# Kernel optimization log

Hardware: AMD Instinct MI355X
Metric: run time of the kernel (lower is better)

## Reference

```python
import jax, jax.numpy as jnp
import numpy as np

B, C, HH, WW, HEADS = 4, 64, 256, 256, 8
CH = C // HEADS              # 8 per-head dim
HID = int(C * 2.66)          # 170
EPS_LN = 1e-5
EPS = 1e-6
QK_NORM = 1.0
# crpe windows for 8 heads: {3:2, 5:3, 7:3}; each conv input split = head_split*Ch*2
WINDOWS = [(3, 2), (5, 3), (7, 3)]


def conv2d(x, w, b=None, groups=1, pad=0):
    out = jax.lax.conv_general_dilated(
        x, w, (1, 1), [(pad, pad), (pad, pad)],
        dimension_numbers=('NCHW', 'OIHW', 'NCHW'), feature_group_count=groups)
    return out if b is None else out + b[None, :, None, None]


def setup_inputs() -> dict:
    key = jax.random.key(0)
    ks = jax.random.split(key, 32)
    p = lambda k, shp, s=0.05: jax.random.normal(k, shp, jnp.float32) * s
    inp = {
        'x': jax.random.normal(ks[0], (B, HH * WW, C), jnp.float32),
        'ln1_w': jnp.ones((C,), jnp.float32) + p(ks[1], (C,), 0.01),
        'sca_w': p(ks[2], (C, C, 1, 1)), 'sca_b': p(ks[3], (C,)),
        'dw1_w': p(ks[4], (2 * C, C, 1, 1)),          # 1x1 dim->2dim
        'dw2_w': p(ks[5], (C, 2, 3, 3)),              # grouped 3x3, groups=C, in/grp=2
        'qkv_w': p(ks[6], (3 * C, C, 1, 1)),
        'qkv_dw_w': p(ks[7], (3 * C, 1, 3, 3)),       # depthwise 3x3
        'temperature': jnp.ones((HEADS, 1, 1), jnp.float32),
        'r3_w': p(ks[8], (2, 2 * CH, 3, 3)), 'r3_b': p(ks[9], (2,)),
        'r5_w': p(ks[10], (3, 2 * CH, 5, 5)), 'r5_b': p(ks[11], (3,)),
        'r7_w': p(ks[12], (3, 2 * CH, 7, 7)), 'r7_b': p(ks[13], (3,)),
        'proj_w': p(ks[14], (C, C, 1, 1)),
        'ln2_w': jnp.ones((C,), jnp.float32) + p(ks[15], (C,), 0.01),
        'pin_w': p(ks[16], (2 * HID, C, 1, 1)),
        'ffn_dw_w': p(ks[17], (2 * HID, 1, 3, 3)),
        'pout_w': p(ks[18], (C, HID, 1, 1)),
        'H': HH, 'W': WW,
    }
    return inp


def biasfree_ln(x, w):
    # BiasFree LayerNorm over channel dim of NCHW (var only, no mean-subtract)
    sigma = jnp.var(x, axis=1, keepdims=True)
    return x / jnp.sqrt(sigma + EPS_LN) * w[None, :, None, None]


def refine_att(q, k, H, W, convs):
    # q: (B,h,N,Ch)  k: (B,h,Ch,N) -> per-head conv relative position map (B,h,N,1)
    b, h, N, Ch = q.shape
    q_img = q.transpose(0, 1, 3, 2).reshape(b, h, Ch, H, W)
    k_img = k.reshape(b, h, Ch, H, W)
    qk = jnp.concatenate([q_img, k_img], axis=2).reshape(b, h * 2 * Ch, H, W)
    splits = np.cumsum([s * 2 * Ch for _, s in WINDOWS])[:-1]
    parts = jnp.split(qk, splits, axis=1)
    outs = [conv2d(xp, wt, bs, groups=g, pad=win // 2)
            for (win, g), (wt, bs), xp in zip(WINDOWS, convs, parts)]
    att = jnp.concatenate(outs, axis=1)           # (b, h, H, W)
    return att.reshape(b, h, 1, H * W).transpose(0, 1, 3, 2)  # (b,h,N,1)


def attention(x, sca_w, sca_b, dw1_w, dw2_w, qkv_w, qkv_dw_w, temperature,
              refine_convs, proj_w, H, W):
    b, c, _, _ = x.shape
    N = H * W
    xsca = conv2d(jnp.mean(x, axis=(2, 3), keepdims=True), sca_w, sca_b)
    x1 = conv2d(conv2d(x, dw1_w), dw2_w, groups=c, pad=1)
    qkv = conv2d(conv2d(x, qkv_w), qkv_dw_w, groups=3 * c, pad=1)
    q, k, v = jnp.split(qkv, 3, axis=1)
    q = q.reshape(b, HEADS, CH, N).transpose(0, 1, 3, 2)  # b h N Ch
    k = k.reshape(b, HEADS, CH, N)                        # b h Ch N
    v = v.reshape(b, HEADS, CH, N).transpose(0, 1, 3, 2)  # b h N Ch
    q = q / (jnp.linalg.norm(q, axis=-1, keepdims=True) / QK_NORM + EPS)
    k = k / (jnp.linalg.norm(k, axis=-2, keepdims=True) / QK_NORM + EPS)
    refine_w = jax.nn.sigmoid(refine_att(q, k, H, W, refine_convs))
    attn = k @ v                                           # b h Ch Ch
    out_num = jnp.sum(v, axis=-2, keepdims=True) + q @ attn
    ksum = jnp.sum(k, axis=-1, keepdims=True)              # b h Ch 1
    out_den = jnp.asarray(N, q.dtype) + q @ ksum + EPS     # b h N 1 (bcast to Ch)
    out = out_num / out_den * temperature
    out = out * refine_w
    out = out.transpose(0, 1, 3, 2).reshape(b, c, H, W)
    out = out * xsca * jax.nn.gelu(x1, approximate=False)
    return conv2d(out, proj_w)


def feedforward(x, pin_w, ffn_dw_w, pout_w):
    h = conv2d(x, pin_w)
    h = conv2d(h, ffn_dw_w, groups=2 * HID, pad=1)
    h1, h2 = jnp.split(h, 2, axis=1)
    return conv2d(jax.nn.gelu(h1, approximate=False) * h2, pout_w)


def reference(x, ln1_w, sca_w, sca_b, dw1_w, dw2_w, qkv_w, qkv_dw_w, temperature,
              r3_w, r3_b, r5_w, r5_b, r7_w, r7_b, proj_w, ln2_w,
              pin_w, ffn_dw_w, pout_w, H, W):
    b = x.shape[0]
    xi = x.reshape(b, H, W, C).transpose(0, 3, 1, 2)  # NCHW
    refine_convs = [(r3_w, r3_b), (r5_w, r5_b), (r7_w, r7_b)]
    xi = xi + attention(biasfree_ln(xi, ln1_w), sca_w, sca_b, dw1_w, dw2_w,
                        qkv_w, qkv_dw_w, temperature, refine_convs, proj_w, H, W)
    xi = xi + feedforward(biasfree_ln(xi, ln2_w), pin_w, ffn_dw_w, pout_w)
    return xi
```

## Files before the change

kernel.cpp:

```cpp
#include <hip/hip_runtime.h>
#include <math.h>
#include <stdio.h>

#define BB 4
#define NP 65536

typedef unsigned short u16;
typedef unsigned int u32;
typedef __attribute__((ext_vector_type(8))) short short8;
typedef __attribute__((ext_vector_type(4))) float f32x4;
typedef __attribute__((ext_vector_type(2))) float f32x2;

__device__ __forceinline__ float bf2f(u16 u) { return __uint_as_float((u32)u << 16); }
__device__ __forceinline__ u16 f2bf(float f) {
  u32 u = __float_as_uint(f);
  u = (u + 0x7FFFu + ((u >> 16) & 1u)) >> 16;
  return (u16)u;
}
__device__ __forceinline__ float gelu_f(float x) {
  return 0.5f * x * (1.f + erff(x * 0.70710678118654752f));
}
__device__ __forceinline__ float wlo(u32 w) { return __uint_as_float(w << 16); }
__device__ __forceinline__ float whi(u32 w) { return __uint_as_float(w & 0xFFFF0000u); }

__global__ __launch_bounds__(256) void k_ln1(const float* __restrict__ x,
                                             u16* __restrict__ xb1,
                                             float* __restrict__ meanraw) {
  int t = threadIdx.x;
  int b = blockIdx.y;
  int lane = t & 63;
  int cg = t & 15;
  float a0 = 0.f, a1 = 0.f, a2 = 0.f, a3 = 0.f;
#pragma unroll
  for (int it = 0; it < 8; it++) {
    long px = (long)blockIdx.x * 128 + (t >> 4) + it * 16;
    const float* xr = x + ((long)b * NP + px) * 64 + cg * 4;
    float4 v = *(const float4*)(xr);
    float s1 = v.x + v.y + v.z + v.w;
    float s2 = v.x * v.x + v.y * v.y + v.z * v.z + v.w * v.w;
    s1 += __shfl_xor(s1, 1); s2 += __shfl_xor(s2, 1);
    s1 += __shfl_xor(s1, 2); s2 += __shfl_xor(s2, 2);
    s1 += __shfl_xor(s1, 4); s2 += __shfl_xor(s2, 4);
    s1 += __shfl_xor(s1, 8); s2 += __shfl_xor(s2, 8);
    float m = s1 * (1.f / 64.f);
    float var = s2 * (1.f / 64.f) - m * m;
    float sg = rsqrtf(var + 1e-5f);
    float h0 = v.x * sg, h1 = v.y * sg, h2 = v.z * sg, h3 = v.w * sg;
    uint2 pk;
    pk.x = (u32)f2bf(h0) | ((u32)f2bf(h1) << 16);
    pk.y = (u32)f2bf(h2) | ((u32)f2bf(h3) << 16);
    *(uint2*)(xb1 + ((long)b * NP + px) * 64 + cg * 4) = pk;
    a0 += h0; a1 += h1; a2 += h2; a3 += h3;
  }
  a0 += __shfl_xor(a0, 16); a1 += __shfl_xor(a1, 16);
  a2 += __shfl_xor(a2, 16); a3 += __shfl_xor(a3, 16);
  a0 += __shfl_xor(a0, 32); a1 += __shfl_xor(a1, 32);
  a2 += __shfl_xor(a2, 32); a3 += __shfl_xor(a3, 32);
  __shared__ float cm[64];
  if (t < 64) cm[t] = 0.f;
  __syncthreads();
  if (lane < 16) {
    atomicAdd(&cm[cg * 4 + 0], a0);
    atomicAdd(&cm[cg * 4 + 1], a1);
    atomicAdd(&cm[cg * 4 + 2], a2);
    atomicAdd(&cm[cg * 4 + 3], a3);
  }
  __syncthreads();
  if (t < 64) atomicAdd(&meanraw[b * 64 + t], cm[t]);
}

__global__ void k_xsca(const float* __restrict__ meanraw, const float* __restrict__ lnw,
                       const float* __restrict__ sca_w, const float* __restrict__ sca_b,
                       float* __restrict__ xsca) {
  int t = threadIdx.x;
  int b = t >> 6, co = t & 63;
  float a = sca_b[co];
  for (int ci = 0; ci < 64; ci++)
    a += sca_w[co * 64 + ci] * meanraw[b * 64 + ci] * lnw[ci] * (1.f / 65536.f);
  xsca[t] = a;
}

__global__ void k_foldW1b(const float* __restrict__ qkv_w, const float* __restrict__ dw1_w,
                          const float* __restrict__ lnw, u16* __restrict__ W1b) {
  int i = blockIdx.x * 256 + threadIdx.x;
  if (i < 320 * 64) {
    int co = i >> 6, ci = i & 63;
    float w = (co < 192) ? qkv_w[co * 64 + ci] : dw1_w[(co - 192) * 64 + ci];
    W1b[i] = f2bf(w * lnw[ci]);
  }
}
__global__ void k_foldW2b(const float* __restrict__ pin_w, const float* __restrict__ lnw,
                          u16* __restrict__ W2b) {
  int i = blockIdx.x * 256 + threadIdx.x;
  if (i < 384 * 64) {
    int co = i >> 6, ci = i & 63;
    float v = 0.f;
    if (co < 340) {
      int pair = co >> 1, which = co & 1;
      v = pin_w[(pair + which * 170) * 64 + ci] * lnw[ci];
    }
    W2b[i] = f2bf(v);
  }
}
__global__ void k_foldWpb(const float* __restrict__ w, u16* __restrict__ Wpb) {
  int i = blockIdx.x * 256 + threadIdx.x;
  if (i < 4096) Wpb[i] = f2bf(w[i]);
}
__global__ void k_tpoutb(const float* __restrict__ w, u16* __restrict__ Wob) {
  int i = blockIdx.x * 256 + threadIdx.x;
  if (i < 64 * 192) {
    int co = i / 192, ci = i - co * 192;
    Wob[i] = (ci < 170) ? f2bf(w[co * 170 + ci]) : (u16)0;
  }
}

template <int EPI>
__global__ __launch_bounds__(256) void k_mgemm(const u16* __restrict__ in, long in_bs,
                                               const u16* __restrict__ W,
                                               u16* __restrict__ outp, long out_bs,
                                               const float* __restrict__ xres,
                                               float* __restrict__ xo,
                                               u16* __restrict__ xb2r) {
  int t = threadIdx.x;
  int lane = t & 63, wv = t >> 6;
  int l15 = lane & 15, quad = lane >> 4;
  int pxw = blockIdx.x * 256 + wv * 64;
  int co0 = blockIdx.y * 64;
  int b = blockIdx.z;
  const u16* inb = in + (long)b * in_bs;

  short8 aw[4][2];
#pragma unroll
  for (int t4 = 0; t4 < 4; t4++)
#pragma unroll
    for (int kf = 0; kf < 2; kf++)
      aw[t4][kf] = *(const short8*)(W + (long)(co0 + t4 * 16 + l15) * 64 + kf * 32 + quad * 8);

  f32x4 acc[4][4];
#pragma unroll
  for (int t4 = 0; t4 < 4; t4++)
#pragma unroll
    for (int p = 0; p < 4; p++) acc[t4][p] = (f32x4){0.f, 0.f, 0.f, 0.f};

#pragma unroll
  for (int p = 0; p < 4; p++) {
    long px = pxw + p * 16 + l15;
    short8 bf0 = *(const short8*)(inb + px * 64 + quad * 8);
    short8 bf1 = *(const short8*)(inb + px * 64 + 32 + quad * 8);
#pragma unroll
    for (int t4 = 0; t4 < 4; t4++) {
      acc[t4][p] = __builtin_amdgcn_mfma_f32_16x16x32_bf16(aw[t4][0], bf0, acc[t4][p], 0, 0, 0);
      acc[t4][p] = __builtin_amdgcn_mfma_f32_16x16x32_bf16(aw[t4][1], bf1, acc[t4][p], 0, 0, 0);
    }
  }

  if (EPI == 0) {
    u16* ob = outp + (long)b * out_bs;
#pragma unroll
    for (int t4 = 0; t4 < 4; t4++)
#pragma unroll
      for (int p = 0; p < 4; p++) {
#pragma unroll
        for (int reg = 0; reg < 4; reg++) {
          int co = co0 + t4 * 16 + quad * 4 + reg;
          ob[(long)co * NP + pxw + p * 16 + l15] = f2bf(acc[t4][p][reg]);
        }
      }
  } else {
#pragma unroll
    for (int p = 0; p < 4; p++) {
      long px = pxw + p * 16 + l15;
      const float* xrow = xres + ((long)b * NP + px) * 64;
      f32x4 xr[4];
#pragma unroll
      for (int t4 = 0; t4 < 4; t4++)
        xr[t4] = *(const f32x4*)(xrow + t4 * 16 + quad * 4);
      float xv[16];
      float s1 = 0.f, s2 = 0.f;
#pragma unroll
      for (int t4 = 0; t4 < 4; t4++)
#pragma unroll
        for (int reg = 0; reg < 4; reg++) {
          float v = xr[t4][reg] + acc[t4][p][reg];
          xv[t4 * 4 + reg] = v;
          s1 += v; s2 += v * v;
        }
      s1 += __shfl_xor(s1, 16); s2 += __shfl_xor(s2, 16);
      s1 += __shfl_xor(s1, 32); s2 += __shfl_xor(s2, 32);
      float m = s1 * (1.f / 64.f);
      float var = s2 * (1.f / 64.f) - m * m;
      float sg = rsqrtf(var + 1e-5f);
#pragma unroll
      for (int t4 = 0; t4 < 4; t4++)
#pragma unroll
        for (int reg = 0; reg < 4; reg++) {
          int co = t4 * 16 + quad * 4 + reg;
          xo[((long)b * 64 + co) * NP + px] = xv[t4 * 4 + reg];
        }
      u16* rp = xb2r + ((long)b * NP + px) * 64;
#pragma unroll
      for (int t4 = 0; t4 < 4; t4++) {
        u32 u0 = (u32)f2bf(xv[t4 * 4 + 0] * sg) | ((u32)f2bf(xv[t4 * 4 + 1] * sg) << 16);
        u32 u1 = (u32)f2bf(xv[t4 * 4 + 2] * sg) | ((u32)f2bf(xv[t4 * 4 + 3] * sg) << 16);
        uint2 pk; pk.x = u0; pk.y = u1;
        *(uint2*)(rp + t4 * 16 + quad * 4) = pk;
      }
    }
  }
}

__device__ __forceinline__ void dw4x2(const u16* __restrict__ img, int y0, int x0, int lane,
                                      const float* __restrict__ w9,
                                      f32x2 o0[2], f32x2 o1[2]) {
  o0[0] = (f32x2){0.f, 0.f}; o0[1] = (f32x2){0.f, 0.f};
  o1[0] = (f32x2){0.f, 0.f}; o1[1] = (f32x2){0.f, 0.f};
#pragma unroll
  for (int r = -1; r <= 2; r++) {
    int row = y0 + r;
    uint2 q; q.x = 0u; q.y = 0u;
    if ((unsigned)row < 256u) q = *(const uint2*)(img + row * 256 + x0);
    u32 qly = (u32)__shfl_up((int)q.y, 1);
    u32 qrx = (u32)__shfl_down((int)q.x, 1);
    if (lane == 0)  qly = 0u;
    if (lane == 63) qrx = 0u;
    float f[6];
    f[0] = whi(qly); f[1] = wlo(q.x); f[2] = whi(q.x);
    f[3] = wlo(q.y); f[4] = whi(q.y); f[5] = wlo(qrx);
    f32x2 fp[5];
#pragma unroll
    for (int i = 0; i < 5; i++) fp[i] = (f32x2){f[i], f[i + 1]};
    if (r <= 1) {
      const float* wr = w9 + (r + 1) * 3;
#pragma unroll
      for (int dx = 0; dx < 3; dx++) {
        f32x2 w2 = {wr[dx], wr[dx]};
        o0[0] += w2 * fp[dx]; o0[1] += w2 * fp[dx + 2];
      }
    }
    if (r >= 0) {
      const float* wr = w9 + r * 3;
#pragma unroll
      for (int dx = 0; dx < 3; dx++) {
        f32x2 w2 = {wr[dx], wr[dx]};
        o1[0] += w2 * fp[dx]; o1[1] += w2 * fp[dx + 2];
      }
    }
  }
}

__global__ __launch_bounds__(256) void k_dwqkv(const u16* __restrict__ P,
                                               const float* __restrict__ dww,
                                               u16* __restrict__ Qn, u16* __restrict__ Kn,
                                               u16* __restrict__ Vn) {
  int t = threadIdx.x;
  int lane = t & 63, wv = t >> 6;
  int by = blockIdx.y;
  int ph = by >> 3, h = by & 7;
  int b = blockIdx.z;
  int y0 = (blockIdx.x * 4 + wv) * 2;
  int x0 = lane * 4;
  int cbase = ph * 64 + h * 8;
  const u16* Pb = P + ((long)b * 192 + cbase) * NP;
  const float* wb = dww + cbase * 9;

  f32x2 v[8][2][2];
#pragma unroll
  for (int c = 0; c < 8; c++)
    dw4x2(Pb + (long)c * NP, y0, x0, lane, wb + c * 9, v[c][0], v[c][1]);

  if (ph < 2) {
#pragma unroll
    for (int row = 0; row < 2; row++) {
      f32x2 s2a = {0.f, 0.f}, s2b = {0.f, 0.f};
#pragma unroll
      for (int c = 0; c < 8; c++) {
        s2a += v[c][row][0] * v[c][row][0];
        s2b += v[c][row][1] * v[c][row][1];
      }
      f32x2 ia, ib;
      ia.x = 1.f / (sqrtf(s2a.x) + 1e-6f); ia.y = 1.f / (sqrtf(s2a.y) + 1e-6f);
      ib.x = 1.f / (sqrtf(s2b.x) + 1e-6f); ib.y = 1.f / (sqrtf(s2b.y) + 1e-6f);
#pragma unroll
      for (int c = 0; c < 8; c++) { v[c][row][0] *= ia; v[c][row][1] *= ib; }
    }
  }
  u16* dst = (ph == 0) ? Qn : (ph == 1) ? Kn : Vn;
#pragma unroll
  for (int c = 0; c < 8; c++)
#pragma unroll
    for (int row = 0; row < 2; row++) {
      ushort4 st;
      st.x = f2bf(v[c][row][0].x); st.y = f2bf(v[c][row][0].y);
      st.z = f2bf(v[c][row][1].x); st.w = f2bf(v[c][row][1].y);
      *(ushort4*)(dst + ((long)b * 64 + h * 8 + c) * NP + (long)(y0 + row) * 256 + x0) = st;
    }
}

__global__ __launch_bounds__(256) void k_stats(const u16* __restrict__ Kn,
                                               const u16* __restrict__ Vn,
                                               float* __restrict__ stats) {
  int t = threadIdx.x;
  int lane = t & 63;
  int h = blockIdx.y, b = blockIdx.z;
  long px = (long)blockIdx.x * 1024 + t * 4;
  const u16* Kb = Kn + ((long)b * 64 + h * 8) * NP + px;
  const u16* Vb = Vn + ((long)b * 64 + h * 8) * NP + px;
  float kf[8][4], vf[8][4];
#pragma unroll
  for (int c = 0; c < 8; c++) {
    ushort4 ku = *(const ushort4*)(Kb + (long)c * NP);
    kf[c][0] = bf2f(ku.x); kf[c][1] = bf2f(ku.y);
    kf[c][2] = bf2f(ku.z); kf[c][3] = bf2f(ku.w);
  }
#pragma unroll
  for (int c = 0; c < 8; c++) {
    ushort4 vu = *(const ushort4*)(Vb + (long)c * NP);
    vf[c][0] = bf2f(vu.x); vf[c][1] = bf2f(vu.y);
    vf[c][2] = bf2f(vu.z); vf[c][3] = bf2f(vu.w);
  }
  __shared__ float sred[80];
  if (t < 80) sred[t] = 0.f;
  __syncthreads();
#pragma unroll
  for (int i = 0; i < 8; i++) {
#pragma unroll
    for (int j = 0; j < 8; j++) {
      float a = kf[i][0] * vf[j][0] + kf[i][1] * vf[j][1] +
                kf[i][2] * vf[j][2] + kf[i][3] * vf[j][3];
      a += __shfl_xor(a, 1); a += __shfl_xor(a, 2); a += __shfl_xor(a, 4);
      a += __shfl_xor(a, 8); a += __shfl_xor(a, 16); a += __shfl_xor(a, 32);
      if (lane == ((i * 8 + j) & 63)) atomicAdd(&sred[i * 8 + j], a);
    }
    {
      float a = kf[i][0] + kf[i][1] + kf[i][2] + kf[i][3];
      a += __shfl_xor(a, 1); a += __shfl_xor(a, 2); a += __shfl_xor(a, 4);
      a += __shfl_xor(a, 8); a += __shfl_xor(a, 16); a += __shfl_xor(a, 32);
      if (lane == ((64 + i) & 63)) atomicAdd(&sred[64 + i], a);
    }
    {
      float a = vf[i][0] + vf[i][1] + vf[i][2] + vf[i][3];
      a += __shfl_xor(a, 1); a += __shfl_xor(a, 2); a += __shfl_xor(a, 4);
      a += __shfl_xor(a, 8); a += __shfl_xor(a, 16); a += __shfl_xor(a, 32);
      if (lane == ((72 + i) & 63)) atomicAdd(&sred[72 + i], a);
    }
  }
  __syncthreads();
  if (t < 80) atomicAdd(&stats[((long)b * 8 + h) * 80 + t], sred[t]);
}

__global__ __launch_bounds__(256) void k_dwg(const u16* __restrict__ P,
                                             const float* __restrict__ dw2_w,
                                             u16* __restrict__ G) {
  int t = threadIdx.x;
  int lane = t & 63, wv = t >> 6;
  int c = blockIdx.y, b = blockIdx.z;
  int y0 = (blockIdx.x * 4 + wv) * 2;
  int x0 = lane * 4;
  const u16* Pb = P + (long)b * 128 * NP;
  f32x2 d1r0[2], d1r1[2], d2r0[2], d2r1[2];
  dw4x2(Pb + (long)(2 * c) * NP, y0, x0, lane, dw2_w + c * 18, d1r0, d1r1);
  dw4x2(Pb + (long)(2 * c + 1) * NP, y0, x0, lane, dw2_w + c * 18 + 9, d2r0, d2r1);
  u16* gp = G + ((long)b * 64 + c) * NP + (long)y0 * 256 + x0;
  ushort4 s0, s1;
  s0.x = f2bf(gelu_f(d1r0[0].x + d2r0[0].x)); s0.y = f2bf(gelu_f(d1r0[0].y + d2r0[0].y));
  s0.z = f2bf(gelu_f(d1r0[1].x + d2r0[1].x)); s0.w = f2bf(gelu_f(d1r0[1].y + d2r0[1].y));
  s1.x = f2bf(gelu_f(d1r1[0].x + d2r1[0].x)); s1.y = f2bf(gelu_f(d1r1[0].y + d2r1[0].y));
  s1.z = f2bf(gelu_f(d1r1[1].x + d2r1[1].x)); s1.w = f2bf(gelu_f(d1r1[1].y + d2r1[1].y));
  *(ushort4*)(gp) = s0;
  *(ushort4*)(gp + 256) = s1;
}

__global__ __launch_bounds__(256) void k_dwgate(const u16* __restrict__ P,
                                                const float* __restrict__ dww,
                                                u16* __restrict__ Hb) {
  int t = threadIdx.x;
  int lane = t & 63, wv = t >> 6;
  int c = blockIdx.y, b = blockIdx.z;
  int y0 = (blockIdx.x * 4 + wv) * 2;
  int x0 = lane * 4;
  const u16* Pb = P + (long)b * 384 * NP;
  f32x2 d1r0[2], d1r1[2], d2r0[2], d2r1[2];
  dw4x2(Pb + (long)(2 * c) * NP, y0, x0, lane, dww + c * 9, d1r0, d1r1);
  dw4x2(Pb + (long)(2 * c + 1) * NP, y0, x0, lane, dww + (170 + c) * 9, d2r0, d2r1);
  u16* hp = Hb + ((long)b * 170 + c) * NP + (long)y0 * 256 + x0;
  ushort4 s0, s1;
  s0.x = f2bf(gelu_f(d1r0[0].x) * d2r0[0].x); s0.y = f2bf(gelu_f(d1r0[0].y) * d2r0[0].y);
  s0.z = f2bf(gelu_f(d1r0[1].x) * d2r0[1].x); s0.w = f2bf(gelu_f(d1r0[1].y) * d2r0[1].y);
  s1.x = f2bf(gelu_f(d1r1[0].x) * d2r1[0].x); s1.y = f2bf(gelu_f(d1r1[0].y) * d2r1[0].y);
  s1.z = f2bf(gelu_f(d1r1[1].x) * d2r1[1].x); s1.w = f2bf(gelu_f(d1r1[1].y) * d2r1[1].y);
  *(ushort4*)(hp) = s0;
  *(ushort4*)(hp + 256) = s1;
}

template <int WIN>
__device__ void refine1(const u16* __restrict__ src, const float* __restrict__ wp,
                        float bias, float* __restrict__ ro, int y0, int x0, int lane) {
  const int R = WIN / 2;
  f32x2 a0a = {bias, bias}, a0b = {bias, bias};
  f32x2 a1a = {bias, bias}, a1b = {bias, bias};
#pragma unroll 1
  for (int ch = 0; ch < 8; ch++) {
    const u16* img = src + (long)ch * NP;
    const float* wc = wp + ch * WIN * WIN;
#pragma unroll
    for (int r = -R; r <= 1 + R; r++) {
      int row = y0 + r;
      uint2 q; q.x = 0u; q.y = 0u;
      if ((unsigned)row < 256u) q = *(const uint2*)(img + row * 256 + x0);
      float f[4 + 2 * R];
      f[R + 0] = wlo(q.x); f[R + 1] = whi(q.x);
      f[R + 2] = wlo(q.y); f[R + 3] = whi(q.y);
      {
        u32 qly = (u32)__shfl_up((int)q.y, 1);
        u32 qrx = (u32)__shfl_down((int)q.x, 1);
        if (lane == 0)  qly = 0u;
        if (lane == 63) qrx = 0u;
        f[R - 1] = whi(qly); f[R + 4] = wlo(qrx);
        if (R >= 2) { f[R - 2] = wlo(qly); f[R + 5] = whi(qrx); }
        if (R >= 3) {
          u32 qlx = (u32)__shfl_up((int)q.x, 1);
          u32 qry = (u32)__shfl_down((int)q.y, 1);
          if (lane == 0)  qlx = 0u;
          if (lane == 63) qry = 0u;
          f[0] = whi(qlx); f[R + 6] = wlo(qry);
        }
      }
      f32x2 fp[3 + 2 * R];
#pragma unroll
      for (int i = 0; i < 3 + 2 * R; i++) fp[i] = (f32x2){f[i], f[i + 1]};
      if (r <= R) {
        const float* w0 = wc + (r + R) * WIN;
#pragma unroll
        for (int dx = 0; dx < WIN; dx++) {
          f32x2 w2 = {w0[dx], w0[dx]};
          a0a += w2 * fp[dx];
          a0b += w2 * fp[dx + 2];
        }
      }
      if (r >= 1 - R) {
        const float* w1 = wc + (r - 1 + R) * WIN;
#pragma unroll
        for (int dx = 0; dx < WIN; dx++) {
          f32x2 w2 = {w1[dx], w1[dx]};
          a1a += w2 * fp[dx];
          a1b += w2 * fp[dx + 2];
        }
      }
    }
  }
  float4 o0, o1;
  o0.x = a0a.x; o0.y = a0a.y; o0.z = a0b.x; o0.w = a0b.y;
  o1.x = a1a.x; o1.y = a1a.y; o1.z = a1b.x; o1.w = a1b.y;
  *(float4*)(ro + (long)y0 * 256 + x0) = o0;
  *(float4*)(ro + (long)(y0 + 1) * 256 + x0) = o1;
}

__global__ __launch_bounds__(256) void k_refine(
    const u16* __restrict__ Qn, const u16* __restrict__ Kn,
    const float* __restrict__ r3w, const float* __restrict__ r3b,
    const float* __restrict__ r5w, const float* __restrict__ r5b,
    const float* __restrict__ r7w, const float* __restrict__ r7b,
    float* __restrict__ refQ, float* __restrict__ refK) {
  int t = threadIdx.x, lane = t & 63, wv = t >> 6;
  int yy = blockIdx.y;
  int h = ((yy >> 1) + 5) & 7;
  int ph = yy & 1;
  int b = blockIdx.z;
  int y0 = (blockIdx.x * 4 + wv) * 2;
  int x0 = lane * 4;
  const u16* src = (ph ? Kn : Qn) + ((long)b * 64 + h * 8) * NP;
  float* ro = (ph ? refK : refQ) + ((long)(b * 8 + h)) * NP;
  if (h < 2) {
    float bias = ph ? 0.f : r3b[h];
    refine1<3>(src, r3w + h * 16 * 9 + ph * 8 * 9, bias, ro, y0, x0, lane);
  } else if (h < 5) {
    float bias = ph ? 0.f : r5b[h - 2];
    refine1<5>(src, r5w + (h - 2) * 16 * 25 + ph * 8 * 25, bias, ro, y0, x0, lane);
  } else {
    float bias = ph ? 0.f : r7b[h - 5];
    refine1<7>(src, r7w + (h - 5) * 16 * 49 + ph * 8 * 49, bias, ro, y0, x0, lane);
  }
}

__global__ __launch_bounds__(256) void k_attn(
    const u16* __restrict__ Qn, const float* __restrict__ stats,
    const float* __restrict__ refQ, const float* __restrict__ refK,
    const float* __restrict__ temp,
    const float* __restrict__ xsca, const u16* __restrict__ G,
    u16* __restrict__ Orows) {
  int b = blockIdx.y;
  int t = threadIdx.x;
  __shared__ float s[640];
  __shared__ float sx[64];
  for (int i = t; i < 640; i += 256) s[i] = stats[(long)b * 640 + i];
  if (t < 64) sx[t] = xsca[b * 64 + t];
  __syncthreads();
  long n = (long)blockIdx.x * 256 + t;
  u16* rp = Orows + ((long)b * NP + n) * 64;
#pragma unroll
  for (int h = 0; h < 8; h++) {
    const float* sh = s + h * 80;
    float q[8];
#pragma unroll
    for (int i = 0; i < 8; i++) q[i] = bf2f(Qn[((long)b * 64 + h * 8 + i) * NP + n]);
    float den = 65536.f + 1e-6f;
#pragma unroll
    for (int i = 0; i < 8; i++) den += q[i] * sh[64 + i];
    float rsum = refQ[((long)(b * 8 + h)) * NP + n] + refK[((long)(b * 8 + h)) * NP + n];
    float tr = temp[h] / ((1.f + expf(-rsum)) * den);
    u32 pk[4];
#pragma unroll
    for (int j2 = 0; j2 < 4; j2++) {
      float o01[2];
#pragma unroll
      for (int e = 0; e < 2; e++) {
        int j = j2 * 2 + e;
        float num = sh[72 + j];
#pragma unroll
        for (int i = 0; i < 8; i++) num += q[i] * sh[i * 8 + j];
        int ci = h * 8 + j;
        o01[e] = num * tr * sx[ci] * bf2f(G[((long)b * 64 + ci) * NP + n]);
      }
      pk[j2] = (u32)f2bf(o01[0]) | ((u32)f2bf(o01[1]) << 16);
    }
    uint4 v; v.x = pk[0]; v.y = pk[1]; v.z = pk[2]; v.w = pk[3];
    *(uint4*)(rp + h * 8) = v;
  }
}

__global__ __launch_bounds__(256) void k_pout(const u16* __restrict__ Hb,
                                              const u16* __restrict__ Wob,
                                              float* __restrict__ xo) {
  __shared__ u16 tile[64 * 196];
  int t = threadIdx.x;
  int lane = t & 63, wv = t >> 6;
  int l15 = lane & 15, quad = lane >> 4;
  int b = blockIdx.z;
  int px0 = blockIdx.x * 64;
  long pxg = px0 + wv * 16 + l15;
  float* xb = xo + (long)b * 64 * NP;

  float res[16];
#pragma unroll
  for (int t4 = 0; t4 < 4; t4++)
#pragma unroll
    for (int reg = 0; reg < 4; reg++) {
      int co = t4 * 16 + quad * 4 + reg;
      res[t4 * 4 + reg] = xb[(long)co * NP + pxg];
    }

  const u16* ib = Hb + (long)b * 170 * NP + px0;
#pragma unroll
  for (int i = 0; i < 6; i++) {
    int task = t + i * 256;
    int ci = task >> 3, pxo = task & 7;
    short8 v = {0, 0, 0, 0, 0, 0, 0, 0};
    if (ci < 170) v = *(const short8*)(ib + (long)ci * NP + pxo * 8);
    const u16* vv = (const u16*)&v;
    u16* dst = tile + (pxo * 8) * 196 + ci;
#pragma unroll
    for (int j = 0; j < 8; j++) dst[j * 196] = vv[j];
  }
  __syncthreads();

  f32x4 acc[4];
#pragma unroll
  for (int t4 = 0; t4 < 4; t4++) acc[t4] = (f32x4){0.f, 0.f, 0.f, 0.f};
  const u16* tb = tile + (wv * 16 + l15) * 196;
#pragma unroll
  for (int kf = 0; kf < 6; kf++) {
    union { uint2 u2[2]; short8 s8; } cv;
    cv.u2[0] = *(const uint2*)(tb + kf * 32 + quad * 8);
    cv.u2[1] = *(const uint2*)(tb + kf * 32 + quad * 8 + 4);
    short8 bfr = cv.s8;
#pragma unroll
    for (int t4 = 0; t4 < 4; t4++) {
      short8 aw = *(const short8*)(Wob + (long)(t4 * 16 + l15) * 192 + kf * 32 + quad * 8);
      acc[t4] = __builtin_amdgcn_mfma_f32_16x16x32_bf16(aw, bfr, acc[t4], 0, 0, 0);
    }
  }
#pragma unroll
  for (int t4 = 0; t4 < 4; t4++)
#pragma unroll
    for (int reg = 0; reg < 4; reg++) {
      int co = t4 * 16 + quad * 4 + reg;
      xb[(long)co * NP + pxg] = res[t4 * 4 + reg] + acc[t4][reg];
    }
}

extern "C" void kernel_launch(void* const* d_in, const int* in_sizes, int n_in,
                              void* d_out, int out_size, void* d_ws, size_t ws_size,
                              hipStream_t stream) {
  const float* x        = (const float*)d_in[0];
  const float* ln1_w    = (const float*)d_in[1];
  const float* sca_w    = (const float*)d_in[2];
  const float* sca_b    = (const float*)d_in[3];
  const float* dw1_w    = (const float*)d_in[4];
  const float* dw2_w    = (const float*)d_in[5];
  const float* qkv_w    = (const float*)d_in[6];
  const float* qkv_dw_w = (const float*)d_in[7];
  const float* temp     = (const float*)d_in[8];
  const float* r3w = (const float*)d_in[9],  *r3b = (const float*)d_in[10];
  const float* r5w = (const float*)d_in[11], *r5b = (const float*)d_in[12];
  const float* r7w = (const float*)d_in[13], *r7b = (const float*)d_in[14];
  const float* proj_w   = (const float*)d_in[15];
  const float* ln2_w    = (const float*)d_in[16];
  const float* pin_w    = (const float*)d_in[17];
  const float* ffn_dw_w = (const float*)d_in[18];
  const float* pout_w   = (const float*)d_in[19];
  float* out = (float*)d_out;
  char* wsb = (char*)d_ws;

  const size_t Mi = 1048576;
  u16* xb1   = (u16*)(wsb);
  u16* Qn    = (u16*)(wsb + 32 * Mi);
  u16* Kn    = (u16*)(wsb + 64 * Mi);
  u16* G     = (u16*)(wsb + 96 * Mi);
  u16* Preg  = (u16*)(wsb + 128 * Mi);
  float* refQ    = (float*)(wsb + 224 * Mi);
  float* refK    = (float*)(wsb + 128 * Mi);
  float* Fm      = (float*)(wsb + 232 * Mi);
  float* stats   = Fm;
  float* meanraw = Fm + 2560;
  float* xscab   = Fm + 2816;
  u16* Wob       = (u16*)(Fm + 3072);
  u16* W1b = (u16*)(Fm + 13952);
  u16* W2b = W1b + 20480;
  u16* Wpb = W2b + 24576;
  u16* xb2 = xb1;
  u16* Orows = Kn;
  u16* Hb = Qn;
  u16* Vn = G;

  const size_t needed = 232 * Mi + 13952 * 4 + (20480 + 24576 + 4096) * 2;
  if (ws_size < needed) {
    fprintf(stderr, "kernel_launch: ws_size %zu < needed %zu\n", ws_size, needed);
    return;
  }

  hipMemsetAsync(stats, 0, (2560 + 256) * 4, stream);
  k_foldW1b<<<80, 256, 0, stream>>>(qkv_w, dw1_w, ln1_w, W1b);
  k_foldW2b<<<96, 256, 0, stream>>>(pin_w, ln2_w, W2b);
  k_foldWpb<<<16, 256, 0, stream>>>(proj_w, Wpb);
  k_tpoutb<<<48, 256, 0, stream>>>(pout_w, Wob);

  k_ln1<<<dim3(512, BB), 256, 0, stream>>>(x, xb1, meanraw);
  k_xsca<<<1, 256, 0, stream>>>(meanraw, ln1_w, sca_w, sca_b, xscab);

  k_mgemm<0><<<dim3(256, 3, BB), 256, 0, stream>>>(xb1, (long)NP * 64, W1b,
                                                   Preg, 192L * NP, nullptr, nullptr, nullptr);
  k_dwqkv<<<dim3(32, 24, BB), 256, 0, stream>>>(Preg, qkv_dw_w, Qn, Kn, Vn);
  k_stats<<<dim3(64, 8, BB), 256, 0, stream>>>(Kn, Vn, stats);

  k_mgemm<0><<<dim3(256, 2, BB), 256, 0, stream>>>(xb1, (long)NP * 64, W1b + 192 * 64,
                                                   Preg, 128L * NP, nullptr, nullptr, nullptr);
  k_dwg<<<dim3(32, 64, BB), 256, 0, stream>>>(Preg, dw2_w, G);

  k_refine<<<dim3(32, 16, BB), 256, 0, stream>>>(Qn, Kn, r3w, r3b, r5w, r5b, r7w, r7b,
                                                 refQ, refK);
  k_attn<<<dim3(256, BB), 256, 0, stream>>>(Qn, stats, refQ, refK, temp, xscab, G, Orows);

  k_mgemm<1><<<dim3(256, 1, BB), 256, 0, stream>>>(Orows, (long)NP * 64, Wpb,
                                                   nullptr, 0, x, out, xb2);

  for (int pass = 0; pass < 2; pass++) {
    k_mgemm<0><<<dim3(256, 6, 2), 256, 0, stream>>>(xb2 + (long)pass * 2 * NP * 64,
                                                    (long)NP * 64, W2b,
                                                    Preg, 384L * NP, nullptr, nullptr, nullptr);
    k_dwgate<<<dim3(32, 170, 2), 256, 0, stream>>>(Preg, ffn_dw_w,
                                                   Hb + (long)pass * 2 * 170 * NP);
  }
  k_pout<<<dim3(1024, 1, BB), 256, 0, stream>>>(Hb, Wob, out);
}
```

Measured before the change: 719.1 us.

## Write FFN gate output pixel-major so output projection skips LDS transpose

The depthwise-gate kernel now processes 32 channels per block and transposes its results through shared memory, storing activations as pixel-major rows with 192 padded channels. The output projection kernel then loads MFMA B fragments directly from global memory with no shared-memory tile or barrier, and each wave computes 64 pixels with a 4x4 accumulator set. The residual is applied by accumulating into the output in place. This trades an extra LDS transpose in the gate kernel and higher register pressure in the projection for contiguous channel access and fewer launches' worth of transpose overhead.

```diff
diff --git a/kernel.cpp b/kernel.cpp
--- a/kernel.cpp
+++ b/kernel.cpp
@@ -370,26 +370,62 @@
   *(ushort4*)(gp + 256) = s1;
 }
 
-__global__ __launch_bounds__(256) void k_dwgate(const u16* __restrict__ P,
-                                                const float* __restrict__ dww,
-                                                u16* __restrict__ Hb) {
+__global__ __launch_bounds__(256) void k_dwgateT(const u16* __restrict__ P,
+                                                 const float* __restrict__ dww,
+                                                 u16* __restrict__ Hrow, int bofs) {
+  __shared__ u16 tile[512 * 36];
   int t = threadIdx.x;
   int lane = t & 63, wv = t >> 6;
-  int c = blockIdx.y, b = blockIdx.z;
-  int y0 = (blockIdx.x * 4 + wv) * 2;
+  int gy = blockIdx.y, b = blockIdx.z;
+  int y0 = blockIdx.x * 2;
   int x0 = lane * 4;
   const u16* Pb = P + (long)b * 384 * NP;
-  f32x2 d1r0[2], d1r1[2], d2r0[2], d2r1[2];
-  dw4x2(Pb + (long)(2 * c) * NP, y0, x0, lane, dww + c * 9, d1r0, d1r1);
-  dw4x2(Pb + (long)(2 * c + 1) * NP, y0, x0, lane, dww + (170 + c) * 9, d2r0, d2r1);
-  u16* hp = Hb + ((long)b * 170 + c) * NP + (long)y0 * 256 + x0;
-  ushort4 s0, s1;
-  s0.x = f2bf(gelu_f(d1r0[0].x) * d2r0[0].x); s0.y = f2bf(gelu_f(d1r0[0].y) * d2r0[0].y);
-  s0.z = f2bf(gelu_f(d1r0[1].x) * d2r0[1].x); s0.w = f2bf(gelu_f(d1r0[1].y) * d2r0[1].y);
-  s1.x = f2bf(gelu_f(d1r1[0].x) * d2r1[0].x); s1.y = f2bf(gelu_f(d1r1[0].y) * d2r1[0].y);
-  s1.z = f2bf(gelu_f(d1r1[1].x) * d2r1[1].x); s1.w = f2bf(gelu_f(d1r1[1].y) * d2r1[1].y);
-  *(ushort4*)(hp) = s0;
-  *(ushort4*)(hp + 256) = s1;
+#pragma unroll 2
+  for (int j8 = 0; j8 < 8; j8++) {
+    int c = gy * 32 + wv * 8 + j8;
+    float H0[4], H1[4];
+    if (c < 170) {
+      f32x2 d1r0[2], d1r1[2], d2r0[2], d2r1[2];
+      dw4x2(Pb + (long)(2 * c) * NP, y0, x0, lane, dww + c * 9, d1r0, d1r1);
+      dw4x2(Pb + (long)(2 * c + 1) * NP, y0, x0, lane, dww + (170 + c) * 9, d2r0, d2r1);
+      H0[0] = gelu_f(d1r0[0].x) * d2r0[0].x; H0[1] = gelu_f(d1r0[0].y) * d2r0[0].y;
+      H0[2] = gelu_f(d1r0[1].x) * d2r0[1].x; H0[3] = gelu_f(d1r0[1].y) * d2r0[1].y;
+      H1[0] = gelu_f(d1r1[0].x) * d2r1[0].x; H1[1] = gelu_f(d1r1[0].y) * d2r1[0].y;
+      H1[2] = gelu_f(d1r1[1].x) * d2r1[1].x; H1[3] = gelu_f(d1r1[1].y) * d2r1[1].y;
+    } else {
+#pragma unroll
+      for (int j = 0; j < 4; j++) { H0[j] = 0.f; H1[j] = 0.f; }
+    }
+    int cc = wv * 8 + j8;
+    int rot = (lane >> 2) & 3;
+#pragma unroll
+    for (int e = 0; e < 8; e++) {
+      int rr = e >> 2;
+      int jj = ((e & 3) + rot) & 3;
+      float v = rr ? H1[jj] : H0[jj];
+      tile[(rr * 256 + x0 + jj) * 36 + cc] = f2bf(v);
+    }
+  }
+  __syncthreads();
+  long gpx0 = (long)(b + bofs) * NP + (long)y0 * 256;
+#pragma unroll
+  for (int pp = 0; pp < 2; pp++) {
+    int lpx = t + pp * 256;
+    const u16* src = tile + lpx * 36;
+    uint2 q0 = *(const uint2*)(src);
+    uint2 q1 = *(const uint2*)(src + 4);
+    uint2 q2 = *(const uint2*)(src + 8);
+    uint2 q3 = *(const uint2*)(src + 12);
+    uint2 q4 = *(const uint2*)(src + 16);
+    uint2 q5 = *(const uint2*)(src + 20);
+    uint2 q6 = *(const uint2*)(src + 24);
+    uint2 q7 = *(const uint2*)(src + 28);
+    u16* dst = Hrow + (gpx0 + lpx) * 192 + gy * 32;
+    *(uint2*)(dst) = q0;      *(uint2*)(dst + 4) = q1;
+    *(uint2*)(dst + 8) = q2;  *(uint2*)(dst + 12) = q3;
+    *(uint2*)(dst + 16) = q4; *(uint2*)(dst + 20) = q5;
+    *(uint2*)(dst + 24) = q6; *(uint2*)(dst + 28) = q7;
+  }
 }
 
 template <int WIN>
@@ -528,64 +564,49 @@
   }
 }
 
-__global__ __launch_bounds__(256) void k_pout(const u16* __restrict__ Hb,
+__global__ __launch_bounds__(256) void k_pout(const u16* __restrict__ Hrow,
                                               const u16* __restrict__ Wob,
                                               float* __restrict__ xo) {
-  __shared__ u16 tile[64 * 196];
   int t = threadIdx.x;
   int lane = t & 63, wv = t >> 6;
   int l15 = lane & 15, quad = lane >> 4;
+  int pxw = blockIdx.x * 256 + wv * 64;
   int b = blockIdx.z;
-  int px0 = blockIdx.x * 64;
-  long pxg = px0 + wv * 16 + l15;
+  const u16* hb = Hrow + (long)b * NP * 192;
+
+  f32x4 acc[4][4];
+#pragma unroll
+  for (int t4 = 0; t4 < 4; t4++)
+#pragma unroll
+    for (int p = 0; p < 4; p++) acc[t4][p] = (f32x4){0.f, 0.f, 0.f, 0.f};
+
+#pragma unroll
+  for (int kf = 0; kf < 6; kf++) {
+    short8 aw[4];
+#pragma unroll
+    for (int t4 = 0; t4 < 4; t4++)
+      aw[t4] = *(const short8*)(Wob + (long)(t4 * 16 + l15) * 192 + kf * 32 + quad * 8);
+#pragma unroll
+    for (int p = 0; p < 4; p++) {
+      long px = pxw + p * 16 + l15;
+      short8 bf = *(const short8*)(hb + px * 192 + kf * 32 + quad * 8);
+#pragma unroll
+      for (int t4 = 0; t4 < 4; t4++)
+        acc[t4][p] = __builtin_amdgcn_mfma_f32_16x16x32_bf16(aw[t4], bf, acc[t4][p], 0, 0, 0);
+    }
+  }
   float* xb = xo + (long)b * 64 * NP;
-
-  float res[16];
-#pragma unroll
-  for (int t4 = 0; t4 < 4; t4++)
-#pragma unroll
-    for (int reg = 0; reg < 4; reg++) {
-      int co = t4 * 16 + quad * 4 + reg;
-      res[t4 * 4 + reg] = xb[(long)co * NP + pxg];
-    }
-
-  const u16* ib = Hb + (long)b * 170 * NP + px0;
-#pragma unroll
-  for (int i = 0; i < 6; i++) {
-    int task = t + i * 256;
-    int ci = task >> 3, pxo = task & 7;
-    short8 v = {0, 0, 0, 0, 0, 0, 0, 0};
-    if (ci < 170) v = *(const short8*)(ib + (long)ci * NP + pxo * 8);
-    const u16* vv = (const u16*)&v;
-    u16* dst = tile + (pxo * 8) * 196 + ci;
-#pragma unroll
-    for (int j = 0; j < 8; j++) dst[j * 196] = vv[j];
-  }
-  __syncthreads();
-
-  f32x4 acc[4];
-#pragma unroll
-  for (int t4 = 0; t4 < 4; t4++) acc[t4] = (f32x4){0.f, 0.f, 0.f, 0.f};
-  const u16* tb = tile + (wv * 16 + l15) * 196;
-#pragma unroll
-  for (int kf = 0; kf < 6; kf++) {
-    union { uint2 u2[2]; short8 s8; } cv;
-    cv.u2[0] = *(const uint2*)(tb + kf * 32 + quad * 8);
-    cv.u2[1] = *(const uint2*)(tb + kf * 32 + quad * 8 + 4);
-    short8 bfr = cv.s8;
-#pragma unroll
-    for (int t4 = 0; t4 < 4; t4++) {
-      short8 aw = *(const short8*)(Wob + (long)(t4 * 16 + l15) * 192 + kf * 32 + quad * 8);
-      acc[t4] = __builtin_amdgcn_mfma_f32_16x16x32_bf16(aw, bfr, acc[t4], 0, 0, 0);
-    }
-  }
-#pragma unroll
-  for (int t4 = 0; t4 < 4; t4++)
-#pragma unroll
-    for (int reg = 0; reg < 4; reg++) {
-      int co = t4 * 16 + quad * 4 + reg;
-      xb[(long)co * NP + pxg] = res[t4 * 4 + reg] + acc[t4][reg];
-    }
+#pragma unroll
+  for (int p = 0; p < 4; p++) {
+    long px = pxw + p * 16 + l15;
+#pragma unroll
+    for (int t4 = 0; t4 < 4; t4++)
+#pragma unroll
+      for (int reg = 0; reg < 4; reg++) {
+        int co = t4 * 16 + quad * 4 + reg;
+        xb[(long)co * NP + px] += acc[t4][p][reg];
+      }
+  }
 }
 
 extern "C" void kernel_launch(void* const* d_in, const int* in_sizes, int n_in,
@@ -619,6 +640,7 @@
   u16* Preg  = (u16*)(wsb + 128 * Mi);
   float* refQ    = (float*)(wsb + 224 * Mi);
   float* refK    = (float*)(wsb + 128 * Mi);
+  u16* Hrow  = Qn;
   float* Fm      = (float*)(wsb + 232 * Mi);
   float* stats   = Fm;
   float* meanraw = Fm + 2560;
@@ -629,7 +651,6 @@
   u16* Wpb = W2b + 24576;
   u16* xb2 = xb1;
   u16* Orows = Kn;
-  u16* Hb = Qn;
   u16* Vn = G;
 
   const size_t needed = 232 * Mi + 13952 * 4 + (20480 + 24576 + 4096) * 2;
@@ -667,8 +688,7 @@
     k_mgemm<0><<<dim3(256, 6, 2), 256, 0, stream>>>(xb2 + (long)pass * 2 * NP * 64,
                                                     (long)NP * 64, W2b,
                                                     Preg, 384L * NP, nullptr, nullptr, nullptr);
-    k_dwgate<<<dim3(32, 170, 2), 256, 0, stream>>>(Preg, ffn_dw_w,
-                                                   Hb + (long)pass * 2 * 170 * NP);
-  }
-  k_pout<<<dim3(1024, 1, BB), 256, 0, stream>>>(Hb, Wob, out);
-}
+    k_dwgateT<<<dim3(128, 6, 2), 256, 0, stream>>>(Preg, ffn_dw_w, Hrow, pass * 2);
+  }
+  k_pout<<<dim3(256, 1, BB), 256, 0, stream>>>(Hrow, Wob, out);
+}
```

Result: slower. 825.6 us (+14.8%).
